# Kernel tuning notes

Hardware: AMD Instinct MI355X
Metric: run time of the kernel (lower is better)

Reference implementation:

```python
import jax, jax.numpy as jnp
import numpy as np

NUM_CLASSES = 10
OUTPUT_DIM = 128
HIDDEN_DIM = 64


def setup_inputs() -> dict:
    key = jax.random.key(0)
    k1, k2, k3, k4, k5, k6 = jax.random.split(key, 6)
    B, S, F = 16, 4096, 512
    X_support = jax.random.normal(k1, (B, S, F), dtype=jnp.float32)
    y_support = jax.random.randint(k2, (B, S), 0, NUM_CLASSES, dtype=jnp.int32)
    # MLP params: Linear(6, HIDDEN) -> GELU -> Linear(HIDDEN, OUTPUT)
    w1 = jax.random.normal(k3, (6, HIDDEN_DIM), dtype=jnp.float32) * (1.0 / np.sqrt(6.0))
    b1 = jax.random.normal(k4, (HIDDEN_DIM,), dtype=jnp.float32) * 0.01
    w2 = jax.random.normal(k5, (HIDDEN_DIM, OUTPUT_DIM), dtype=jnp.float32) * (1.0 / np.sqrt(HIDDEN_DIM))
    b2 = jax.random.normal(k6, (OUTPUT_DIM,), dtype=jnp.float32) * 0.01
    return {"X_support": X_support, "y_support": y_support,
            "w1": w1, "b1": b1, "w2": w2, "b2": b2}


def _feature_target_stats(X, y):
    """Vectorized equivalent of FeatureTargetStatsEncoder per-(batch,feature) loops.
    X: [B, S, F] float, y: [B, S] int class labels. Returns stats [B, F, 6]."""
    B, S, F = X.shape
    missing_rate = jnp.isnan(X).astype(X.dtype).mean(axis=1)           # [B, F]
    Xc = jnp.nan_to_num(X, nan=0.0)
    gmean = Xc.mean(axis=1)                                            # [B, F]
    variance = Xc.var(axis=1)                                          # biased (unbiased=False)
    absX = jnp.abs(Xc)
    mean_abs = absX.mean(axis=1)
    max_abs = absX.max(axis=1)
    # unique_ratio: count distinct values per (b, f) via sort + diff
    xs = jnp.sort(Xc, axis=1)
    n_unique = 1.0 + (jnp.diff(xs, axis=1) != 0).astype(Xc.dtype).sum(axis=1)
    unique_ratio = n_unique / S
    # classification target score: between-class variance / overall variance
    onehot = jax.nn.one_hot(y, NUM_CLASSES, dtype=Xc.dtype)            # [B, S, C]
    counts = onehot.sum(axis=1)                                        # [B, C]
    csum = jnp.einsum('bsc,bsf->bcf', onehot, Xc)                      # [B, C, F]
    cmean = csum / jnp.maximum(counts, 1.0)[:, :, None]
    dev2 = (cmean - gmean[:, None, :]) ** 2
    between = (counts[:, :, None] * dev2).sum(axis=1) / jnp.maximum(counts.sum(axis=1), 1.0)[:, None]
    target_score = between / jnp.maximum(variance, 1e-6)
    stats = jnp.stack([target_score, missing_rate, unique_ratio,
                       variance, mean_abs, max_abs], axis=-1)          # [B, F, 6]
    return jnp.nan_to_num(stats, nan=0.0, posinf=0.0, neginf=0.0)


def reference(X_support, y_support, w1, b1, w2, b2):
    stats = _feature_target_stats(X_support, y_support)                # [B, F, 6]
    h = jax.nn.gelu(stats @ w1 + b1, approximate=False)               # exact GELU like nn.GELU()
    return h @ w2 + b2                                                 # [B, F, OUTPUT_DIM]
```

## Files before the change

kernel.cpp:

```cpp
#include <hip/hip_runtime.h>
#include <math.h>

#define NS 4096
#define NF 512
#define NB 16
#define NC 10
#define HSIZE 8192
#define HMASK 8191
#define HEMPTY 0xFFFFFFFFu

__global__ void count_classes_kernel(const int* __restrict__ y, float* __restrict__ counts) {
    __shared__ int hist[NC];
    const int b = blockIdx.x;
    if (threadIdx.x < NC) hist[threadIdx.x] = 0;
    __syncthreads();
    for (int s = threadIdx.x; s < NS; s += blockDim.x)
        atomicAdd(&hist[y[b * NS + s]], 1);
    __syncthreads();
    if (threadIdx.x < NC) counts[b * NC + threadIdx.x] = (float)hist[threadIdx.x];
}

__device__ __forceinline__ float wave_reduce_add(float v) {
    #pragma unroll
    for (int off = 32; off > 0; off >>= 1) v += __shfl_down(v, off, 64);
    return v;
}
__device__ __forceinline__ float wave_reduce_max(float v) {
    #pragma unroll
    for (int off = 32; off > 0; off >>= 1) v = fmaxf(v, __shfl_down(v, off, 64));
    return v;
}

__launch_bounds__(256)
__global__ void fused_stats_mlp_kernel(const float* __restrict__ X,
                                       const int* __restrict__ y,
                                       const float* __restrict__ counts,
                                       const float* __restrict__ w1,
                                       const float* __restrict__ b1,
                                       const float* __restrict__ w2,
                                       const float* __restrict__ b2,
                                       float* __restrict__ out) {
    __shared__ unsigned int hash[HSIZE];
    __shared__ float red[4][16];
    __shared__ float stats_s[6];
    __shared__ float h_s[64];

    const int w = blockIdx.x;
    const int g = (w & 7) * 1024 + (w >> 3);
    const int b = g >> 9;
    const int f = g & (NF - 1);
    const int tid = threadIdx.x;

    #pragma unroll
    for (int i = 0; i < HSIZE / 256; i++) hash[tid + i * 256] = HEMPTY;
    __syncthreads();

    const float* Xp = X + (size_t)b * NS * NF + f;
    const int*   yp = y + b * NS;

    float sum = 0.f, sumsq = 0.f, sumabs = 0.f, maxabs = 0.f, nancnt = 0.f, uniq = 0.f;
    float csum[NC];
    #pragma unroll
    for (int c = 0; c < NC; c++) csum[c] = 0.f;

    #pragma unroll
    for (int k0 = 0; k0 < 16; k0 += 8) {
        float xv[8]; int yv[8];
        #pragma unroll
        for (int k = 0; k < 8; k++) {
            const int s = (k0 + k) * 256 + tid;
            xv[k] = Xp[(size_t)s * NF];
            yv[k] = yp[s];
        }
        #pragma unroll
        for (int k = 0; k < 8; k++) {
            float x = xv[k];
            if (x != x) { nancnt += 1.f; x = 0.f; }
            sum += x;
            sumsq = fmaf(x, x, sumsq);
            const float a = fabsf(x);
            sumabs += a;
            maxabs = fmaxf(maxabs, a);
            const int yc = yv[k];
            #pragma unroll
            for (int c = 0; c < NC; c++) csum[c] += (yc == c) ? x : 0.f;
            unsigned int pat = __float_as_uint(x);
            if (pat == 0x80000000u) pat = 0u;
            unsigned int slot = (pat * 2654435761u) >> 19;
            for (;;) {
                const unsigned int old = atomicCAS(&hash[slot], HEMPTY, pat);
                if (old == HEMPTY) { uniq += 1.f; break; }
                if (old == pat) break;
                slot = (slot + 1) & HMASK;
            }
        }
    }

    sum    = wave_reduce_add(sum);
    sumsq  = wave_reduce_add(sumsq);
    sumabs = wave_reduce_add(sumabs);
    nancnt = wave_reduce_add(nancnt);
    uniq   = wave_reduce_add(uniq);
    maxabs = wave_reduce_max(maxabs);
    #pragma unroll
    for (int c = 0; c < NC; c++) csum[c] = wave_reduce_add(csum[c]);

    const int wave = tid >> 6, lane = tid & 63;
    if (lane == 0) {
        red[wave][0] = sum;    red[wave][1] = sumsq; red[wave][2] = sumabs;
        red[wave][3] = nancnt; red[wave][4] = uniq;  red[wave][5] = maxabs;
        #pragma unroll
        for (int c = 0; c < NC; c++) red[wave][6 + c] = csum[c];
    }
    __syncthreads();

    if (tid == 0) {
        float t[16];
        #pragma unroll
        for (int v = 0; v < 16; v++) t[v] = red[0][v];
        #pragma unroll
        for (int wv = 1; wv < 4; wv++) {
            #pragma unroll
            for (int v = 0; v < 16; v++) {
                if (v == 5) t[v] = fmaxf(t[v], red[wv][v]);
                else        t[v] += red[wv][v];
            }
        }
        const float invS = 1.f / (float)NS;
        const float gmean    = t[0] * invS;
        const float variance = fmaxf(t[1] * invS - gmean * gmean, 0.f);
        const float mean_abs = t[2] * invS;
        const float missing  = t[3] * invS;
        const float n_unique = t[4];
        const float max_abs  = t[5];
        float between = 0.f;
        #pragma unroll
        for (int c = 0; c < NC; c++) {
            const float cnt = counts[b * NC + c];
            const float cm  = t[6 + c] / fmaxf(cnt, 1.f);
            const float d   = cm - gmean;
            between += cnt * d * d;
        }
        between *= invS;
        const float target = between / fmaxf(variance, 1e-6f);
        float st[6] = { target, missing, n_unique * invS, variance, mean_abs, max_abs };
        #pragma unroll
        for (int i = 0; i < 6; i++) {
            float v = st[i];
            if (!(fabsf(v) < INFINITY)) v = 0.f;
            stats_s[i] = v;
        }
    }
    __syncthreads();

    if (tid < 64) {
        float z = b1[tid];
        #pragma unroll
        for (int i = 0; i < 6; i++) z = fmaf(stats_s[i], w1[i * 64 + tid], z);
        h_s[tid] = 0.5f * z * (1.f + erff(z * 0.70710678118654752440f));
    }
    __syncthreads();
    if (tid < 128) {
        float o = b2[tid];
        #pragma unroll
        for (int j = 0; j < 64; j++) o = fmaf(h_s[j], w2[j * 128 + tid], o);
        out[(size_t)g * 128 + tid] = o;
    }
}

extern "C" void kernel_launch(void* const* d_in, const int* in_sizes, int n_in,
                              void* d_out, int out_size, void* d_ws, size_t ws_size,
                              hipStream_t stream) {
    const float* X  = (const float*)d_in[0];
    const int*   y  = (const int*)d_in[1];
    const float* w1 = (const float*)d_in[2];
    const float* b1 = (const float*)d_in[3];
    const float* w2 = (const float*)d_in[4];
    const float* b2 = (const float*)d_in[5];
    float* out    = (float*)d_out;
    float* counts = (float*)d_ws;

    count_classes_kernel<<<NB, 256, 0, stream>>>(y, counts);
    fused_stats_mlp_kernel<<<NB * NF, 256, 0, stream>>>(X, y, counts, w1, b1, w2, b2, out);
}
```

Before: 353.9 us.

## Split moment stats into coalesced pass and vectorize unique-count hashing over four features

The single fused per-feature kernel is split into two. A coalesced row-streaming pass accumulates sums, max and per-class sums with global atomics. A second kernel handles four features per block, loading each row as one float4 into four shared hash tables for distinct-value counting, then runs the MLP for each feature. The aim is to replace strided single-float loads (one feature per block) with coalesced and vector loads, reading X twice instead of once. The costs are a memset, float atomics whose order is nondeterministic, and 128KB of shared memory per block, which limits occupancy.

```diff
diff --git a/kernel.cpp b/kernel.cpp
--- a/kernel.cpp
+++ b/kernel.cpp
@@ -5,166 +5,189 @@
 #define NF 512
 #define NB 16
 #define NC 10
-#define HSIZE 8192
+#define HS 8192
 #define HMASK 8191
 #define HEMPTY 0xFFFFFFFFu
 
-__global__ void count_classes_kernel(const int* __restrict__ y, float* __restrict__ counts) {
+#define STATS_BYTES (NB * NF * 16 * 4)
+
+__global__ void count_classes_kernel(const int* __restrict__ y, int* __restrict__ counts) {
     __shared__ int hist[NC];
-    const int b = blockIdx.x;
+    const int b = blockIdx.x >> 3;
+    const int chunk = blockIdx.x & 7;
     if (threadIdx.x < NC) hist[threadIdx.x] = 0;
     __syncthreads();
-    for (int s = threadIdx.x; s < NS; s += blockDim.x)
+    const int s0 = chunk * 512;
+    for (int s = s0 + threadIdx.x; s < s0 + 512; s += 256)
         atomicAdd(&hist[y[b * NS + s]], 1);
     __syncthreads();
-    if (threadIdx.x < NC) counts[b * NC + threadIdx.x] = (float)hist[threadIdx.x];
-}
-
-__device__ __forceinline__ float wave_reduce_add(float v) {
+    if (threadIdx.x < NC) atomicAdd(&counts[b * NC + threadIdx.x], hist[threadIdx.x]);
+}
+
+__launch_bounds__(256)
+__global__ void stats_pass_kernel(const float* __restrict__ X,
+                                  const int* __restrict__ y,
+                                  float* __restrict__ statsb) {
+    const int w  = blockIdx.x;
+    const int b  = w >> 5;
+    const int sc = (w >> 1) & 15;
+    const int fh = w & 1;
+    const int f  = fh * 256 + threadIdx.x;
+
+    const float* Xp = X + ((size_t)b * NS + (size_t)sc * 256) * NF + f;
+    const int*   yp = y + b * NS + sc * 256;
+
+    float sum = 0.f, sumsq = 0.f, sumabs = 0.f, nancnt = 0.f, maxab = 0.f;
+    float cs[NC];
+    #pragma unroll
+    for (int c = 0; c < NC; c++) cs[c] = 0.f;
+
+    #pragma unroll 4
+    for (int r = 0; r < 256; ++r) {
+        float x = Xp[(size_t)r * NF];
+        const int yv = __builtin_amdgcn_readfirstlane(yp[r]);
+        if (x != x) { nancnt += 1.f; x = 0.f; }
+        sum += x;
+        sumsq = fmaf(x, x, sumsq);
+        const float a = fabsf(x);
+        sumabs += a;
+        maxab = fmaxf(maxab, a);
+        #pragma unroll
+        for (int c = 0; c < NC; c++)
+            if (yv == c) cs[c] += x;
+    }
+
+    float* sp = statsb + ((size_t)(b * NF + f)) * 16;
+    atomicAdd(sp + 0, sum);
+    atomicAdd(sp + 1, sumsq);
+    atomicAdd(sp + 2, sumabs);
+    atomicAdd(sp + 3, nancnt);
+    atomicMax((int*)(sp + 4), __float_as_int(maxab));
+    #pragma unroll
+    for (int c = 0; c < NC; c++) atomicAdd(sp + 5 + c, cs[c]);
+}
+
+__device__ __forceinline__ int wave_reduce_add_i(int v) {
     #pragma unroll
     for (int off = 32; off > 0; off >>= 1) v += __shfl_down(v, off, 64);
     return v;
 }
-__device__ __forceinline__ float wave_reduce_max(float v) {
-    #pragma unroll
-    for (int off = 32; off > 0; off >>= 1) v = fmaxf(v, __shfl_down(v, off, 64));
-    return v;
+
+__device__ __forceinline__ void hash_insert(unsigned int* hbase, float x, int& u) {
+    if (x != x) x = 0.f;
+    unsigned int pat = __float_as_uint(x);
+    if (pat == 0x80000000u) pat = 0u;
+    unsigned int slot = (pat * 2654435761u) >> 19;
+    for (;;) {
+        const unsigned int old = atomicCAS(hbase + slot, HEMPTY, pat);
+        if (old == HEMPTY) { u++; break; }
+        if (old == pat) break;
+        slot = (slot + 1) & HMASK;
+    }
 }
 
 __launch_bounds__(256)
-__global__ void fused_stats_mlp_kernel(const float* __restrict__ X,
-                                       const int* __restrict__ y,
-                                       const float* __restrict__ counts,
-                                       const float* __restrict__ w1,
-                                       const float* __restrict__ b1,
-                                       const float* __restrict__ w2,
-                                       const float* __restrict__ b2,
-                                       float* __restrict__ out) {
-    __shared__ unsigned int hash[HSIZE];
-    __shared__ float red[4][16];
-    __shared__ float stats_s[6];
+__global__ void unique_mlp_kernel(const float* __restrict__ X,
+                                  const float* __restrict__ statsb,
+                                  const int* __restrict__ counts,
+                                  const float* __restrict__ w1,
+                                  const float* __restrict__ b1,
+                                  const float* __restrict__ w2,
+                                  const float* __restrict__ b2,
+                                  float* __restrict__ out) {
+    __shared__ unsigned int hash[4][HS];
+    __shared__ float sld[4][16];
+    __shared__ float cld[NC];
+    __shared__ int   redu[4][4];
+    __shared__ float st_s[6];
     __shared__ float h_s[64];
 
-    const int w = blockIdx.x;
-    const int g = (w & 7) * 1024 + (w >> 3);
-    const int b = g >> 9;
-    const int f = g & (NF - 1);
+    const int w  = blockIdx.x;
+    const int g4 = (w & 7) * 256 + (w >> 3);
+    const int b  = g4 >> 7;
+    const int f0 = (g4 << 2) & (NF - 1);
     const int tid = threadIdx.x;
 
-    #pragma unroll
-    for (int i = 0; i < HSIZE / 256; i++) hash[tid + i * 256] = HEMPTY;
-    __syncthreads();
-
-    const float* Xp = X + (size_t)b * NS * NF + f;
-    const int*   yp = y + b * NS;
-
-    float sum = 0.f, sumsq = 0.f, sumabs = 0.f, maxabs = 0.f, nancnt = 0.f, uniq = 0.f;
-    float csum[NC];
-    #pragma unroll
-    for (int c = 0; c < NC; c++) csum[c] = 0.f;
-
-    #pragma unroll
-    for (int k0 = 0; k0 < 16; k0 += 8) {
-        float xv[8]; int yv[8];
+    uint4* hp = (uint4*)&hash[0][0];
+    #pragma unroll
+    for (int i = 0; i < (4 * HS / 4) / 256; i++)
+        hp[tid + i * 256] = make_uint4(HEMPTY, HEMPTY, HEMPTY, HEMPTY);
+    if (tid < 64) ((float*)sld)[tid] = statsb[(size_t)g4 * 64 + tid];
+    if (tid >= 64 && tid < 64 + NC) cld[tid - 64] = (float)counts[b * NC + (tid - 64)];
+    __syncthreads();
+
+    const float* Xb = X + ((size_t)b * NS) * NF + f0;
+    int uniq[4] = {0, 0, 0, 0};
+
+    #pragma unroll
+    for (int i0 = 0; i0 < 16; i0 += 4) {
+        float4 v[4];
         #pragma unroll
-        for (int k = 0; k < 8; k++) {
-            const int s = (k0 + k) * 256 + tid;
-            xv[k] = Xp[(size_t)s * NF];
-            yv[k] = yp[s];
+        for (int k = 0; k < 4; k++) {
+            const int s = (i0 + k) * 256 + tid;
+            v[k] = *(const float4*)(Xb + (size_t)s * NF);
         }
         #pragma unroll
-        for (int k = 0; k < 8; k++) {
-            float x = xv[k];
-            if (x != x) { nancnt += 1.f; x = 0.f; }
-            sum += x;
-            sumsq = fmaf(x, x, sumsq);
-            const float a = fabsf(x);
-            sumabs += a;
-            maxabs = fmaxf(maxabs, a);
-            const int yc = yv[k];
-            #pragma unroll
-            for (int c = 0; c < NC; c++) csum[c] += (yc == c) ? x : 0.f;
-            unsigned int pat = __float_as_uint(x);
-            if (pat == 0x80000000u) pat = 0u;
-            unsigned int slot = (pat * 2654435761u) >> 19;
-            for (;;) {
-                const unsigned int old = atomicCAS(&hash[slot], HEMPTY, pat);
-                if (old == HEMPTY) { uniq += 1.f; break; }
-                if (old == pat) break;
-                slot = (slot + 1) & HMASK;
+        for (int k = 0; k < 4; k++) {
+            hash_insert(hash[0], v[k].x, uniq[0]);
+            hash_insert(hash[1], v[k].y, uniq[1]);
+            hash_insert(hash[2], v[k].z, uniq[2]);
+            hash_insert(hash[3], v[k].w, uniq[3]);
+        }
+    }
+
+    const int wave = tid >> 6, lane = tid & 63;
+    #pragma unroll
+    for (int c = 0; c < 4; c++) {
+        const int u = wave_reduce_add_i(uniq[c]);
+        if (lane == 0) redu[wave][c] = u;
+    }
+    __syncthreads();
+
+    const float invS = 1.f / (float)NS;
+    #pragma unroll
+    for (int c = 0; c < 4; c++) {
+        if (tid == 0) {
+            const float n_unique = (float)(redu[0][c] + redu[1][c] + redu[2][c] + redu[3][c]);
+            const float sum      = sld[c][0];
+            const float gmean    = sum * invS;
+            const float variance = fmaxf(sld[c][1] * invS - gmean * gmean, 0.f);
+            const float mean_abs = sld[c][2] * invS;
+            const float missing  = sld[c][3] * invS;
+            const float max_abs  = sld[c][4];
+            float between = 0.f;
+            #pragma unroll
+            for (int cc = 0; cc < NC; cc++) {
+                const float cnt = cld[cc];
+                const float cm  = sld[c][5 + cc] / fmaxf(cnt, 1.f);
+                const float d   = cm - gmean;
+                between += cnt * d * d;
             }
-        }
-    }
-
-    sum    = wave_reduce_add(sum);
-    sumsq  = wave_reduce_add(sumsq);
-    sumabs = wave_reduce_add(sumabs);
-    nancnt = wave_reduce_add(nancnt);
-    uniq   = wave_reduce_add(uniq);
-    maxabs = wave_reduce_max(maxabs);
-    #pragma unroll
-    for (int c = 0; c < NC; c++) csum[c] = wave_reduce_add(csum[c]);
-
-    const int wave = tid >> 6, lane = tid & 63;
-    if (lane == 0) {
-        red[wave][0] = sum;    red[wave][1] = sumsq; red[wave][2] = sumabs;
-        red[wave][3] = nancnt; red[wave][4] = uniq;  red[wave][5] = maxabs;
-        #pragma unroll
-        for (int c = 0; c < NC; c++) red[wave][6 + c] = csum[c];
-    }
-    __syncthreads();
-
-    if (tid == 0) {
-        float t[16];
-        #pragma unroll
-        for (int v = 0; v < 16; v++) t[v] = red[0][v];
-        #pragma unroll
-        for (int wv = 1; wv < 4; wv++) {
-            #pragma unroll
-            for (int v = 0; v < 16; v++) {
-                if (v == 5) t[v] = fmaxf(t[v], red[wv][v]);
-                else        t[v] += red[wv][v];
+            between *= invS;
+            const float target = between / fmaxf(variance, 1e-6f);
+            float st[6] = { target, missing, n_unique * invS, variance, mean_abs, max_abs };
+            #pragma unroll
+            for (int i = 0; i < 6; i++) {
+                float vv = st[i];
+                if (!(fabsf(vv) < INFINITY)) vv = 0.f;
+                st_s[i] = vv;
             }
         }
-        const float invS = 1.f / (float)NS;
-        const float gmean    = t[0] * invS;
-        const float variance = fmaxf(t[1] * invS - gmean * gmean, 0.f);
-        const float mean_abs = t[2] * invS;
-        const float missing  = t[3] * invS;
-        const float n_unique = t[4];
-        const float max_abs  = t[5];
-        float between = 0.f;
-        #pragma unroll
-        for (int c = 0; c < NC; c++) {
-            const float cnt = counts[b * NC + c];
-            const float cm  = t[6 + c] / fmaxf(cnt, 1.f);
-            const float d   = cm - gmean;
-            between += cnt * d * d;
-        }
-        between *= invS;
-        const float target = between / fmaxf(variance, 1e-6f);
-        float st[6] = { target, missing, n_unique * invS, variance, mean_abs, max_abs };
-        #pragma unroll
-        for (int i = 0; i < 6; i++) {
-            float v = st[i];
-            if (!(fabsf(v) < INFINITY)) v = 0.f;
-            stats_s[i] = v;
-        }
-    }
-    __syncthreads();
-
-    if (tid < 64) {
-        float z = b1[tid];
-        #pragma unroll
-        for (int i = 0; i < 6; i++) z = fmaf(stats_s[i], w1[i * 64 + tid], z);
-        h_s[tid] = 0.5f * z * (1.f + erff(z * 0.70710678118654752440f));
-    }
-    __syncthreads();
-    if (tid < 128) {
-        float o = b2[tid];
-        #pragma unroll
-        for (int j = 0; j < 64; j++) o = fmaf(h_s[j], w2[j * 128 + tid], o);
-        out[(size_t)g * 128 + tid] = o;
+        __syncthreads();
+        if (tid < 64) {
+            float z = b1[tid];
+            #pragma unroll
+            for (int i = 0; i < 6; i++) z = fmaf(st_s[i], w1[i * 64 + tid], z);
+            h_s[tid] = 0.5f * z * (1.f + erff(z * 0.70710678118654752440f));
+        }
+        __syncthreads();
+        if (tid < 128) {
+            float o = b2[tid];
+            #pragma unroll
+            for (int j = 0; j < 64; j++) o = fmaf(h_s[j], w2[j * 128 + tid], o);
+            out[((size_t)(g4 * 4 + c)) * 128 + tid] = o;
+        }
+        __syncthreads();
     }
 }
 
@@ -177,9 +200,12 @@
     const float* b1 = (const float*)d_in[3];
     const float* w2 = (const float*)d_in[4];
     const float* b2 = (const float*)d_in[5];
-    float* out    = (float*)d_out;
-    float* counts = (float*)d_ws;
-
-    count_classes_kernel<<<NB, 256, 0, stream>>>(y, counts);
-    fused_stats_mlp_kernel<<<NB * NF, 256, 0, stream>>>(X, y, counts, w1, b1, w2, b2, out);
-}
+    float* out     = (float*)d_out;
+    float* statsb  = (float*)d_ws;
+    int*   counts  = (int*)((char*)d_ws + STATS_BYTES);
+
+    hipMemsetAsync(d_ws, 0, STATS_BYTES + NB * NC * 4, stream);
+    count_classes_kernel<<<NB * 8, 256, 0, stream>>>(y, counts);
+    stats_pass_kernel<<<NB * 16 * 2, 256, 0, stream>>>(X, y, statsb);
+    unique_mlp_kernel<<<NB * NF / 4, 256, 0, stream>>>(X, statsb, counts, w1, b1, w2, b2, out);
+}
```

Result: slower. 717.8 us (+102.8%).
